# Kernel optimization log

Measured on AMD Instinct MI355X. Metric: run time of the kernel, lower is better.

Reference implementation:

```python
import jax, jax.numpy as jnp
import numpy as np

SPECIES = (0, 1)
CUTOFF = 6.0
N_ATOMS, N_EDGES, N_TRIPLETS = 20000, 500000, 2000000

G2_ETAS = np.array([0.003214, 0.035711, 0.071421, 0.124987, 0.214264, 0.357106, 0.714213, 1.428426], dtype=np.float32)
G4_ETAS = np.array([0.000357, 0.028569, 0.089277], dtype=np.float32)
G4_ZETAS = np.array([1.0, 2.0, 4.0], dtype=np.float32)
G4_LMDAS = np.array([-1.0, 1.0], dtype=np.float32)


def setup_inputs() -> dict:
    key = jax.random.key(0)
    ks = jax.random.split(key, 6)
    atomic_numbers = jax.random.randint(ks[0], (N_ATOMS,), 0, 2, dtype=jnp.int32)
    edge_index = jax.random.randint(ks[1], (2, N_EDGES), 0, N_ATOMS, dtype=jnp.int32)
    D_st = jax.random.uniform(ks[2], (N_EDGES,), minval=0.5, maxval=6.5, dtype=jnp.float32)
    id3_ba = jax.random.randint(ks[3], (N_TRIPLETS,), 0, N_EDGES, dtype=jnp.int32)
    id3_ca = jax.random.randint(ks[4], (N_TRIPLETS,), 0, N_EDGES, dtype=jnp.int32)
    cosphi = jax.random.uniform(ks[5], (N_TRIPLETS,), minval=-1.0, maxval=1.0, dtype=jnp.float32)
    # per-key parameters: 4 ordered species pairs for G2, 6 species triples for G4
    g2_etas = jnp.tile(jnp.asarray(G2_ETAS), (4, 1))
    g4_etas = jnp.tile(jnp.asarray(G4_ETAS), (6, 1))
    g4_zetas = jnp.tile(jnp.asarray(G4_ZETAS), (6, 1))
    g4_lmdas = jnp.tile(jnp.asarray(G4_LMDAS), (6, 1))
    return {"atomic_numbers": atomic_numbers, "edge_index": edge_index, "D_st": D_st,
            "id3_ba": id3_ba, "id3_ca": id3_ca, "cosphi": cosphi,
            "g2_etas": g2_etas, "g4_etas": g4_etas, "g4_zetas": g4_zetas, "g4_lmdas": g4_lmdas}


def _fc(R):
    # cosine cutoff (no in-range bool here; G4 applies its own range masks)
    return 0.5 * jnp.cos(jnp.pi * R / CUTOFF) + 0.5


def _acsf(atomic_numbers, edge_index, D_st, id3_ba, id3_ca, cosphi,
          g2_etas, g4_etas, g4_zetas, g4_lmdas):
    N = atomic_numbers.shape[0]
    dt = D_st.dtype
    src, tgt = edge_index[0], edge_index[1]
    an_src, an_tgt = atomic_numbers[src], atomic_numbers[tgt]

    # ---- triplet geometry (masking replaces boolean gather; scatter-add is equivalent) ----
    m3 = id3_ba > id3_ca                       # [T] triplet dedup mask
    R_ba = D_st[id3_ba]                        # [T]
    R_ca = D_st[id3_ca]
    sb = atomic_numbers[src[id3_ba]]           # species of edge-ba source
    tb = atomic_numbers[tgt[id3_ba]]           # species of central atom a
    sc = atomic_numbers[src[id3_ca]]
    seg3 = tgt[id3_ba]                         # scatter target: central atom index
    Rbc2 = R_ba * R_ba + R_ca * R_ca - 2.0 * R_ba * R_ca * cosphi
    R_bc = jnp.sqrt(jnp.maximum(Rbc2, 1e-12))
    in_range = ((R_bc < CUTOFF) & (R_ba < CUTOFF) & (R_ca < CUTOFF)).astype(dt)
    cut3 = _fc(R_ca) * _fc(R_bc) * _fc(R_ba) * in_range   # [T]
    r2sum = R_bc * R_bc + R_ba * R_ba + R_ca * R_ca       # [T]

    # ---- G2: per (source, target) species pair ----
    cut2 = _fc(D_st)                           # [E]
    d2 = D_st * D_st
    g2_per = {}
    k = 0
    for a1 in SPECIES:
        for a2 in SPECIES:
            w = ((an_tgt == a2) & (an_src == a1)).astype(dt)       # [E]
            res = (cut2 * w)[:, None] * jnp.exp(-g2_etas[k][None, :] * d2[:, None])  # [E,8]
            g2_per[(a1, a2)] = jax.ops.segment_sum(res, tgt, num_segments=N)        # [N,8]
            k += 1

    # ---- G4: per (a, b, c) species triple (b<=c) ----
    ns = len(SPECIES)
    g4_per = {}
    k = 0
    for a in SPECIES:
        for i in range(ns):
            b = SPECIES[i]
            for j in range(i, ns):
                c = SPECIES[j]
                idx = (((sb == b) & (tb == a) & (sc == c)) |
                       ((sb == c) & (tb == a) & (sc == b)))
                w = (m3 & idx).astype(dt)                                  # [T]
                eta, zta, lmda = g4_etas[k], g4_zetas[k], g4_lmdas[k]
                rad = jnp.exp(-eta[None, :] * r2sum[:, None])              # [T,3]
                cl = jnp.abs(1.0 + lmda[None, :, None] * cosphi[:, None, None]) ** zta[None, None, :]  # [T,2,3]
                res = cl[:, None, :, :] * rad[:, :, None, None] * (cut3 * w)[:, None, None, None]      # [T,3,2,3]
                g4 = jax.ops.segment_sum(res, seg3, num_segments=N)        # [N,3,2,3]
                g4_per[(a, b, c)] = (2.0 ** (1.0 - zta))[None, None, None, :] * g4
                k += 1

    # ---- assemble per-atom descriptor [N, 70]; rows carry their species' descriptor ----
    outs = []
    for a in SPECIES:
        mask = (atomic_numbers == a).astype(dt)[:, None]
        g2s = jnp.stack([g2_per[(s, a)] for s in SPECIES], axis=-1).reshape(N, -1)   # [N,16]
        trips = [(b, c) for i, b in enumerate(SPECIES) for c in SPECIES[i:]]
        g4s = jnp.stack([g4_per[(a, b, c)] for (b, c) in trips], axis=-1).reshape(N, -1)  # [N,54]
        outs.append(mask * jnp.concatenate([g2s, g4s], axis=-1))
    return outs[0] + outs[1]


def reference(atomic_numbers, edge_index, D_st, id3_ba, id3_ca, cosphi,
              g2_etas, g4_etas, g4_zetas, g4_lmdas):
    return _acsf(atomic_numbers, edge_index, D_st, id3_ba, id3_ca, cosphi,
                 g2_etas, g4_etas, g4_zetas, g4_lmdas)
```

## Files before the change

kernel.cpp:

```cpp
#include <hip/hip_runtime.h>


#define CAP_T 96
#define CAP_E 64

typedef int    vi2 __attribute__((ext_vector_type(2)));
typedef int    vi4 __attribute__((ext_vector_type(4)));
typedef float  vf2 __attribute__((ext_vector_type(2)));
typedef float  vf4 __attribute__((ext_vector_type(4)));

static __device__ __forceinline__ float fc_dev(float R) {
    const float PI_OVER_CUT = 0.52359877559829887308f;
    return fmaf(0.5f, __cosf(PI_OVER_CUT * R), 0.5f);
}

static __device__ __forceinline__ unsigned enc_R(float d) {
    float u = rintf(d * (65535.0f / 8.0f));
    u = fminf(fmaxf(u, 0.0f), 65535.0f);
    return (unsigned)u;
}
static __device__ __forceinline__ float dec_R(unsigned pk) {
    return (float)(pk >> 16) * (8.0f / 65535.0f);
}


static __device__ __forceinline__ void process_edge(
        int e, float d, int src, int tgt,
        const int* __restrict__ an, const float* __restrict__ g2_etas,
        unsigned* __restrict__ epack, int* __restrict__ ecount,
        unsigned* __restrict__ erec, float* __restrict__ out) {
    int as = an[src];
    unsigned dq = enc_R(d);
    epack[e] = (dq << 16) | ((unsigned)tgt << 1) | (unsigned)as;
    float fcv = fc_dev(d);
    int slot = atomicAdd(&ecount[tgt], 1);
    if (slot < CAP_E) {
        unsigned fq = (unsigned)rintf(fminf(fmaxf(fcv, 0.0f), 1.0f) * 32767.0f);
        erec[(size_t)tgt * CAP_E + slot] = (dq << 16) | (fq << 1) | (unsigned)as;
    } else {
        float d2 = d * d;
        int at = an[tgt];
        const float* eta = g2_etas + (as * 2 + at) * 8;
        float* row = out + (size_t)tgt * 70 + as;
#pragma unroll
        for (int i = 0; i < 8; ++i)
            atomicAdd(row + 2 * i, fcv * __expf(-eta[i] * d2));
    }
}

__global__ void edges_bin_kernel(const int* __restrict__ an,
                                 const int* __restrict__ ei,
                                 const float* __restrict__ D,
                                 const float* __restrict__ g2_etas,
                                 unsigned* __restrict__ epack,
                                 int* __restrict__ ecount,
                                 unsigned* __restrict__ erec,
                                 float* __restrict__ out, int E) {
    int i = blockIdx.x * blockDim.x + threadIdx.x;
    int e0 = i * 2;
    if (e0 >= E) return;
    if (e0 + 1 < E) {
        vi2 sp = __builtin_nontemporal_load((const vi2*)ei + i);
        vi2 tp = __builtin_nontemporal_load((const vi2*)(ei + E) + i);
        vf2 dp = __builtin_nontemporal_load((const vf2*)D + i);
        process_edge(e0,     dp.x, sp.x, tp.x, an, g2_etas, epack, ecount, erec, out);
        process_edge(e0 + 1, dp.y, sp.y, tp.y, an, g2_etas, epack, ecount, erec, out);
    } else {
        process_edge(e0, D[e0], ei[e0], ei[E + e0], an, g2_etas, epack, ecount,
                     erec, out);
    }
}

static __device__ __forceinline__ void process_triplet(
        unsigned pb, unsigned pc, float cph,
        const int* __restrict__ an,
        const float* __restrict__ g4_etas,
        const float* __restrict__ g4_zetas,
        const float* __restrict__ g4_lmdas,
        int* __restrict__ tcount, vf2* __restrict__ trec,
        float* __restrict__ out) {
    float R_ba = dec_R(pb);
    float R_ca = dec_R(pc);
    if (R_ba >= 6.0f || R_ca >= 6.0f) return;
    float Rbc2 = R_ba * R_ba + R_ca * R_ca - 2.0f * R_ba * R_ca * cph;
    float Rm2 = fmaxf(Rbc2, 1e-12f);
    float R_bc = sqrtf(Rm2);
    if (R_bc >= 6.0f) return;
    int seg = (int)((pb >> 1) & 0x7FFFu);
    int trip = (int)(pb & 1u) + (int)(pc & 1u);
    float cut3 = fc_dev(R_ba) * fc_dev(R_ca) * fc_dev(R_bc);
    float r2sum = Rm2 + R_ba * R_ba + R_ca * R_ca;
    int slot = atomicAdd(&tcount[seg], 1);
    if (slot < CAP_T) {
        float cqf = fminf(fmaxf(fmaf(cph, 32767.5f, 32767.5f), 0.0f), 65535.0f);
        unsigned cq = (unsigned)rintf(cqf);
        unsigned c3q = (unsigned)rintf(cut3 * 16383.0f);
        unsigned w0 = (cq << 16) | (c3q << 2) | (unsigned)trip;
        vf2 r; r.x = __uint_as_float(w0); r.y = r2sum;
        trec[(size_t)seg * CAP_T + slot] = r;
    } else {
        int A = an[seg];
        int k4 = A * 3 + trip;
        const float* eta = g4_etas + k4 * 3;
        const float* zet = g4_zetas + k4 * 3;
        const float* lmd = g4_lmdas + k4 * 2;
        float rad[3];
#pragma unroll
        for (int e2 = 0; e2 < 3; ++e2)
            rad[e2] = __expf(-eta[e2] * r2sum) * cut3;
        float lg0 = __log2f(fabsf(fmaf(lmd[0], cph, 1.0f)));
        float lg1 = __log2f(fabsf(fmaf(lmd[1], cph, 1.0f)));
        float* row = out + (size_t)seg * 70 + 16 + trip;
#pragma unroll
        for (int z = 0; z < 3; ++z) {
            float zv = zet[z], base = 1.0f - zv;
            float c0 = exp2f(fmaf(zv, lg0, base));
            float c1 = exp2f(fmaf(zv, lg1, base));
#pragma unroll
            for (int e2 = 0; e2 < 3; ++e2) {
                atomicAdd(row + ((e2 * 2 + 0) * 3 + z) * 3, c0 * rad[e2]);
                atomicAdd(row + ((e2 * 2 + 1) * 3 + z) * 3, c1 * rad[e2]);
            }
        }
    }
}

__global__ void trip_bin_kernel(const unsigned* __restrict__ epack,
                                const int* __restrict__ id3_ba,
                                const int* __restrict__ id3_ca,
                                const float* __restrict__ cosphi,
                                const int* __restrict__ an,
                                const float* __restrict__ g4_etas,
                                const float* __restrict__ g4_zetas,
                                const float* __restrict__ g4_lmdas,
                                int* __restrict__ tcount,
                                vf2* __restrict__ trec,
                                float* __restrict__ out, int T) {
    int i = blockIdx.x * blockDim.x + threadIdx.x;
    int t0 = i * 4;
    if (t0 >= T) return;
    int ba[4], ca[4];
    float cp[4];
    if (t0 + 3 < T) {
        vi4 b4 = __builtin_nontemporal_load((const vi4*)id3_ba + i);
        vi4 c4 = __builtin_nontemporal_load((const vi4*)id3_ca + i);
        vf4 p4 = __builtin_nontemporal_load((const vf4*)cosphi + i);
        ba[0] = b4.x; ba[1] = b4.y; ba[2] = b4.z; ba[3] = b4.w;
        ca[0] = c4.x; ca[1] = c4.y; ca[2] = c4.z; ca[3] = c4.w;
        cp[0] = p4.x; cp[1] = p4.y; cp[2] = p4.z; cp[3] = p4.w;
    } else {
#pragma unroll
        for (int k = 0; k < 4; ++k) {
            int t = t0 + k;
            ba[k] = (t < T) ? id3_ba[t] : 0;
            ca[k] = (t < T) ? id3_ca[t] : 0;
            cp[k] = (t < T) ? cosphi[t] : 0.0f;
        }
    }
    unsigned pb[4], pc[4];
    bool m[4];
#pragma unroll
    for (int k = 0; k < 4; ++k) {
        m[k] = ba[k] > ca[k];
        pb[k] = 0u; pc[k] = 0u;
        if (m[k]) {
            pb[k] = epack[ba[k]];
            pc[k] = epack[ca[k]];
        }
    }
#pragma unroll
    for (int k = 0; k < 4; ++k) {
        if (m[k])
            process_triplet(pb[k], pc[k], cp[k], an, g4_etas, g4_zetas,
                            g4_lmdas, tcount, trec, out);
    }
}

__global__ __launch_bounds__(256) void gather_kernel(
        const int* __restrict__ an,
        const float* __restrict__ g2_etas,
        const float* __restrict__ g4_etas,
        const float* __restrict__ g4_zetas,
        const float* __restrict__ g4_lmdas,
        const int* __restrict__ tcount, const vf2* __restrict__ trec,
        const int* __restrict__ ecount, const unsigned* __restrict__ erec,
        float* __restrict__ out, int N) {
    __shared__ vf2      sg4[4][66];
    __shared__ unsigned sg2[4][64];
    int w = threadIdx.x >> 6;
    int lane = threadIdx.x & 63;
    int a = blockIdx.x * 4 + w;
    if (a >= N) return;
    int A = an[a];

    int c18 = lane % 18;
    int g3  = lane / 18;
    int g3r = (g3 > 2) ? 0 : g3;
    int z_c = c18 % 3;
    int l_c = (c18 / 3) % 2;
    int e_c = c18 / 6;
    float eta0, eta1, eta2w, zv0, zv1, zv2, lm0, lm1, lm2;
    {
        int k0 = A * 3 + 0, k1 = A * 3 + 1, k2 = A * 3 + 2;
        eta0 = g4_etas[k0 * 3 + e_c]; eta1 = g4_etas[k1 * 3 + e_c]; eta2w = g4_etas[k2 * 3 + e_c];
        zv0  = g4_zetas[k0 * 3 + z_c]; zv1 = g4_zetas[k1 * 3 + z_c]; zv2 = g4_zetas[k2 * 3 + z_c];
        lm0  = g4_lmdas[k0 * 2 + l_c]; lm1 = g4_lmdas[k1 * 2 + l_c]; lm2 = g4_lmdas[k2 * 2 + l_c];
    }
    auto zsel = [](float z) -> int {
        return (z == 1.0f) ? 0 : (z == 2.0f) ? 1 : (z == 4.0f) ? 2 : 3;
    };
    int zs0 = zsel(zv0), zs1 = zsel(zv1), zs2 = zsel(zv2);
    bool fastz = __all(zs0 < 3 && zs1 < 3 && zs2 < 3);

    int n_t = min(tcount[a], CAP_T);
    const vf2* rec = trec + (size_t)a * CAP_T;
    float acc0 = 0.0f, acc1 = 0.0f, acc2 = 0.0f;
    vf2 zr; zr.x = 0.0f; zr.y = 0.0f;
    for (int b0 = 0; b0 < n_t; b0 += 64) {
        int nch = min(64, n_t - b0);
        vf2 rv = zr;
        if (lane < nch) rv = __builtin_nontemporal_load(rec + b0 + lane);
        sg4[w][lane] = rv;
        if (lane < 2) sg4[w][64 + lane] = zr;
        asm volatile("s_waitcnt lgkmcnt(0)" ::: "memory");
        int niter = (nch + 2) / 3;
        if (fastz) {
            for (int i = 0; i < niter; ++i) {
                vf2 b = sg4[w][i * 3 + g3r];
                unsigned w0 = __float_as_uint(b.x);
                int btr = (int)(w0 & 3u);
                float cut3 = (float)((w0 >> 2) & 0x3FFFu) * (1.0f / 16383.0f);
                float c = fmaf((float)(w0 >> 16), 2.0f / 65535.0f, -1.0f);
                float eta_r = (btr == 0) ? eta0 : (btr == 1) ? eta1 : eta2w;
                float lm_r  = (btr == 0) ? lm0  : (btr == 1) ? lm1  : lm2;
                int   zs_r  = (btr == 0) ? zs0  : (btr == 1) ? zs1  : zs2;
                float p1 = fabsf(fmaf(lm_r, c, 1.0f));
                float p2 = p1 * p1;
                float p4 = p2 * p2;
                float cl = (zs_r == 0) ? p1 : (zs_r == 1) ? p2 * 0.5f : p4 * 0.125f;
                float v = cl * __expf(-eta_r * b.y) * cut3;
                acc0 += (btr == 0) ? v : 0.0f;
                acc1 += (btr == 1) ? v : 0.0f;
                acc2 += (btr == 2) ? v : 0.0f;
            }
        } else {
            for (int i = 0; i < niter; ++i) {
                vf2 b = sg4[w][i * 3 + g3r];
                unsigned w0 = __float_as_uint(b.x);
                int btr = (int)(w0 & 3u);
                float cut3 = (float)((w0 >> 2) & 0x3FFFu) * (1.0f / 16383.0f);
                float c = fmaf((float)(w0 >> 16), 2.0f / 65535.0f, -1.0f);
                float eta_r = (btr == 0) ? eta0 : (btr == 1) ? eta1 : eta2w;
                float lm_r  = (btr == 0) ? lm0  : (btr == 1) ? lm1  : lm2;
                float zv_r  = (btr == 0) ? zv0  : (btr == 1) ? zv1  : zv2;
                float p1 = fabsf(fmaf(lm_r, c, 1.0f));
                float cl = exp2f(fmaf(zv_r, __log2f(p1), 1.0f - zv_r));
                float v = cl * __expf(-eta_r * b.y) * cut3;
                acc0 += (btr == 0) ? v : 0.0f;
                acc1 += (btr == 1) ? v : 0.0f;
                acc2 += (btr == 2) ? v : 0.0f;
            }
        }
    }
    {
        int cc = lane / 3;
        int tt = lane - cc * 3;
        float s0a = __shfl(acc0, cc),      s1a = __shfl(acc1, cc),      s2a = __shfl(acc2, cc);
        float s0b = __shfl(acc0, cc + 18), s1b = __shfl(acc1, cc + 18), s2b = __shfl(acc2, cc + 18);
        float s0c = __shfl(acc0, cc + 36), s1c = __shfl(acc1, cc + 36), s2c = __shfl(acc2, cc + 36);
        float va = (tt == 0) ? s0a : (tt == 1) ? s1a : s2a;
        float vb = (tt == 0) ? s0b : (tt == 1) ? s1b : s2b;
        float vc = (tt == 0) ? s0c : (tt == 1) ? s1c : s2c;
        if (lane < 54) out[(size_t)a * 70 + 16 + lane] += va + vb + vc;
    }

    int c16 = lane & 15;
    int g4g = lane >> 4;
    int s_c = c16 & 1;
    int i_c = c16 >> 1;
    float eta2 = g2_etas[(s_c * 2 + A) * 8 + i_c];
    int n_e = min(ecount[a], CAP_E);
    const unsigned* erc = erec + (size_t)a * CAP_E;
    float accg = 0.0f;
    for (int b0 = 0; b0 < n_e; b0 += 64) {
        int nch = min(64, n_e - b0);
        unsigned rv = 0u;
        if (lane < nch) rv = __builtin_nontemporal_load(erc + b0 + lane);
        sg2[w][lane] = rv;
        asm volatile("s_waitcnt lgkmcnt(0)" ::: "memory");
        int niter = (nch + 3) / 4;
        for (int i = 0; i < niter; ++i) {
            unsigned pk = sg2[w][i * 4 + g4g];
            int sp = (int)(pk & 1u);
            float d = dec_R(pk);
            float fcv = (float)((pk >> 1) & 0x7FFFu) * (1.0f / 32767.0f);
            float v = fcv * __expf(-eta2 * d * d);
            accg += (sp == s_c) ? v : 0.0f;
        }
    }
    {
        float r0 = __shfl(accg, lane);
        float r1 = __shfl(accg, lane + 16);
        float r2 = __shfl(accg, lane + 32);
        float r3 = __shfl(accg, lane + 48);
        if (lane < 16) out[(size_t)a * 70 + lane] += r0 + r1 + r2 + r3;
    }
}


__global__ void acsf_edges_kernel(const int* __restrict__ an,
                                  const int* __restrict__ ei,
                                  const float* __restrict__ D,
                                  const float* __restrict__ g2_etas,
                                  float2* __restrict__ edata,
                                  float* __restrict__ out,
                                  int E, int use_ws) {
    int e = blockIdx.x * blockDim.x + threadIdx.x;
    if (e >= E) return;
    float d = D[e];
    float cut2 = fc_dev(d);
    if (use_ws) edata[e] = make_float2(d, cut2);
    int src = ei[e];
    int tgt = ei[E + e];
    int as = an[src];
    int at = an[tgt];
    float d2 = d * d;
    const float* eta = g2_etas + (as * 2 + at) * 8;
    float* row = out + (size_t)tgt * 70 + as;
#pragma unroll
    for (int i = 0; i < 8; ++i)
        atomicAdd(row + 2 * i, cut2 * __expf(-eta[i] * d2));
}

__global__ void acsf_triplets_kernel(const int* __restrict__ an,
                                     const int* __restrict__ ei,
                                     const float* __restrict__ D,
                                     const float2* __restrict__ edata,
                                     const int* __restrict__ id3_ba,
                                     const int* __restrict__ id3_ca,
                                     const float* __restrict__ cosphi,
                                     const float* __restrict__ g4_etas,
                                     const float* __restrict__ g4_zetas,
                                     const float* __restrict__ g4_lmdas,
                                     float* __restrict__ out,
                                     int T, int E, int use_ws) {
    int t = blockIdx.x * blockDim.x + threadIdx.x;
    if (t >= T) return;
    int eba = id3_ba[t];
    int eca = id3_ca[t];
    if (eba <= eca) return;
    float R_ba, R_ca, fba, fca;
    if (use_ws) {
        float2 va = edata[eba];
        float2 vb = edata[eca];
        R_ba = va.x; fba = va.y;
        R_ca = vb.x; fca = vb.y;
    } else {
        R_ba = D[eba]; R_ca = D[eca];
        fba = fc_dev(R_ba); fca = fc_dev(R_ca);
    }
    if (R_ba >= 6.0f || R_ca >= 6.0f) return;
    float cph = cosphi[t];
    float Rbc2 = R_ba * R_ba + R_ca * R_ca - 2.0f * R_ba * R_ca * cph;
    float Rm2 = fmaxf(Rbc2, 1e-12f);
    float R_bc = sqrtf(Rm2);
    if (R_bc >= 6.0f) return;
    int seg = ei[E + eba];
    int A = an[seg];
    int sb = an[ei[eba]];
    int sc = an[ei[eca]];
    int trip = sb + sc;
    int k4 = A * 3 + trip;
    float cut3 = fba * fca * fc_dev(R_bc);
    float r2sum = Rm2 + R_ba * R_ba + R_ca * R_ca;
    const float* eta = g4_etas + k4 * 3;
    const float* zet = g4_zetas + k4 * 3;
    const float* lmd = g4_lmdas + k4 * 2;
    float rad[3];
#pragma unroll
    for (int e2 = 0; e2 < 3; ++e2)
        rad[e2] = __expf(-eta[e2] * r2sum) * cut3;
    float lg0 = __log2f(fabsf(fmaf(lmd[0], cph, 1.0f)));
    float lg1 = __log2f(fabsf(fmaf(lmd[1], cph, 1.0f)));
    float* row = out + (size_t)seg * 70 + 16 + trip;
#pragma unroll
    for (int z = 0; z < 3; ++z) {
        float zv = zet[z], bse = 1.0f - zv;
        float c0 = exp2f(fmaf(zv, lg0, bse));
        float c1 = exp2f(fmaf(zv, lg1, bse));
#pragma unroll
        for (int e2 = 0; e2 < 3; ++e2) {
            atomicAdd(row + ((e2 * 2 + 0) * 3 + z) * 3, c0 * rad[e2]);
            atomicAdd(row + ((e2 * 2 + 1) * 3 + z) * 3, c1 * rad[e2]);
        }
    }
}


extern "C" void kernel_launch(void* const* d_in, const int* in_sizes, int n_in,
                              void* d_out, int out_size, void* d_ws, size_t ws_size,
                              hipStream_t stream) {
    const int*   an       = (const int*)d_in[0];
    const int*   ei       = (const int*)d_in[1];
    const float* D        = (const float*)d_in[2];
    const int*   id3_ba   = (const int*)d_in[3];
    const int*   id3_ca   = (const int*)d_in[4];
    const float* cosphi   = (const float*)d_in[5];
    const float* g2_etas  = (const float*)d_in[6];
    const float* g4_etas  = (const float*)d_in[7];
    const float* g4_zetas = (const float*)d_in[8];
    const float* g4_lmdas = (const float*)d_in[9];
    (void)n_in;

    int N = in_sizes[0];
    int E = in_sizes[2];
    int T = in_sizes[3];
    float* out = (float*)d_out;

    size_t trec_b  = (size_t)N * CAP_T * sizeof(vf2);
    size_t epack_b = (size_t)((E + 1) & ~1) * sizeof(unsigned);
    size_t erec_b  = (size_t)N * CAP_E * sizeof(unsigned);
    size_t cnt_b   = (size_t)N * sizeof(int) * 2;
    size_t need = trec_b + epack_b + erec_b + cnt_b;

    const int blk = 256;
    (void)hipMemsetAsync(d_out, 0, (size_t)out_size * sizeof(float), stream);

    if (ws_size >= need && N <= 32767) {
        char* p = (char*)d_ws;
        vf2*      trec  = (vf2*)p;             p += trec_b;
        unsigned* epack = (unsigned*)p;        p += epack_b;
        unsigned* erec  = (unsigned*)p;        p += erec_b;
        int*      tcount = (int*)p;
        int*      ecount = tcount + N;
        (void)hipMemsetAsync(tcount, 0, cnt_b, stream);

        int ethreads = (E + 1) / 2;
        edges_bin_kernel<<<(ethreads + blk - 1) / blk, blk, 0, stream>>>(
            an, ei, D, g2_etas, epack, ecount, erec, out, E);
        int tthreads = (T + 3) / 4;
        trip_bin_kernel<<<(tthreads + blk - 1) / blk, blk, 0, stream>>>(
            epack, id3_ba, id3_ca, cosphi, an,
            g4_etas, g4_zetas, g4_lmdas, tcount, trec, out, T);
        gather_kernel<<<(N + 3) / 4, blk, 0, stream>>>(
            an, g2_etas, g4_etas, g4_zetas, g4_lmdas,
            tcount, trec, ecount, erec, out, N);
    } else {
        int use_ws = (ws_size >= (size_t)E * sizeof(float2)) ? 1 : 0;
        float2* edata = (float2*)d_ws;
        acsf_edges_kernel<<<(E + blk - 1) / blk, blk, 0, stream>>>(
            an, ei, D, g2_etas, edata, out, E, use_ws);
        acsf_triplets_kernel<<<(T + blk - 1) / blk, blk, 0, stream>>>(
            an, ei, D, edata, id3_ba, id3_ca, cosphi,
            g4_etas, g4_zetas, g4_lmdas, out, T, E, use_ws);
    }
}
```

Baseline: 186.6 us.

## Shard per-atom triplet and edge bins across eight block-indexed shards

Splits the per-atom bin counters and record arrays into eight shards chosen by block index, so atomics on the same atom's counter contend less and records spread over more memory. The gather kernel sums the per-shard counts and maps each lane's record index to a shard and local slot before loading. The binning kernels now compute geometry for all four triplets and issue their atomics together to expose more memory-level parallelism. Per-shard capacity is small (16), so more records may spill to the slow direct-atomic path on busy shards. Gather also does eight counter loads and extra index arithmetic per atom.

New measurement: 188.5 us. No clear change (+1.0%).

```diff
diff --git a/kernel.cpp b/kernel.cpp
--- a/kernel.cpp
+++ b/kernel.cpp
@@ -1,13 +1,15 @@
 #include <hip/hip_runtime.h>
 
 
-#define CAP_T 96
-#define CAP_E 64
-
-typedef int    vi2 __attribute__((ext_vector_type(2)));
-typedef int    vi4 __attribute__((ext_vector_type(4)));
-typedef float  vf2 __attribute__((ext_vector_type(2)));
-typedef float  vf4 __attribute__((ext_vector_type(4)));
+#define NSH    8
+#define CAP_TS 16
+#define CAP_ES 16
+
+typedef int      vi2 __attribute__((ext_vector_type(2)));
+typedef int      vi4 __attribute__((ext_vector_type(4)));
+typedef float    vf2 __attribute__((ext_vector_type(2)));
+typedef float    vf4 __attribute__((ext_vector_type(4)));
+typedef unsigned vu2 __attribute__((ext_vector_type(2)));
 
 static __device__ __forceinline__ float fc_dev(float R) {
     const float PI_OVER_CUT = 0.52359877559829887308f;
@@ -23,30 +25,6 @@
     return (float)(pk >> 16) * (8.0f / 65535.0f);
 }
 
-
-static __device__ __forceinline__ void process_edge(
-        int e, float d, int src, int tgt,
-        const int* __restrict__ an, const float* __restrict__ g2_etas,
-        unsigned* __restrict__ epack, int* __restrict__ ecount,
-        unsigned* __restrict__ erec, float* __restrict__ out) {
-    int as = an[src];
-    unsigned dq = enc_R(d);
-    epack[e] = (dq << 16) | ((unsigned)tgt << 1) | (unsigned)as;
-    float fcv = fc_dev(d);
-    int slot = atomicAdd(&ecount[tgt], 1);
-    if (slot < CAP_E) {
-        unsigned fq = (unsigned)rintf(fminf(fmaxf(fcv, 0.0f), 1.0f) * 32767.0f);
-        erec[(size_t)tgt * CAP_E + slot] = (dq << 16) | (fq << 1) | (unsigned)as;
-    } else {
-        float d2 = d * d;
-        int at = an[tgt];
-        const float* eta = g2_etas + (as * 2 + at) * 8;
-        float* row = out + (size_t)tgt * 70 + as;
-#pragma unroll
-        for (int i = 0; i < 8; ++i)
-            atomicAdd(row + 2 * i, fcv * __expf(-eta[i] * d2));
-    }
-}
 
 __global__ void edges_bin_kernel(const int* __restrict__ an,
                                  const int* __restrict__ ei,
@@ -55,72 +33,64 @@
                                  unsigned* __restrict__ epack,
                                  int* __restrict__ ecount,
                                  unsigned* __restrict__ erec,
-                                 float* __restrict__ out, int E) {
+                                 float* __restrict__ out, int E, int N) {
+    int shard = blockIdx.x & (NSH - 1);
+    int* __restrict__ ecnt = ecount + (size_t)shard * N;
     int i = blockIdx.x * blockDim.x + threadIdx.x;
     int e0 = i * 2;
     if (e0 >= E) return;
+
+    int   srcs[2], tgts[2];
+    float ds[2];
+    int   nk;
     if (e0 + 1 < E) {
         vi2 sp = __builtin_nontemporal_load((const vi2*)ei + i);
         vi2 tp = __builtin_nontemporal_load((const vi2*)(ei + E) + i);
         vf2 dp = __builtin_nontemporal_load((const vf2*)D + i);
-        process_edge(e0,     dp.x, sp.x, tp.x, an, g2_etas, epack, ecount, erec, out);
-        process_edge(e0 + 1, dp.y, sp.y, tp.y, an, g2_etas, epack, ecount, erec, out);
+        srcs[0] = sp.x; srcs[1] = sp.y;
+        tgts[0] = tp.x; tgts[1] = tp.y;
+        ds[0] = dp.x;   ds[1] = dp.y;
+        nk = 2;
     } else {
-        process_edge(e0, D[e0], ei[e0], ei[E + e0], an, g2_etas, epack, ecount,
-                     erec, out);
-    }
-}
-
-static __device__ __forceinline__ void process_triplet(
-        unsigned pb, unsigned pc, float cph,
-        const int* __restrict__ an,
-        const float* __restrict__ g4_etas,
-        const float* __restrict__ g4_zetas,
-        const float* __restrict__ g4_lmdas,
-        int* __restrict__ tcount, vf2* __restrict__ trec,
-        float* __restrict__ out) {
-    float R_ba = dec_R(pb);
-    float R_ca = dec_R(pc);
-    if (R_ba >= 6.0f || R_ca >= 6.0f) return;
-    float Rbc2 = R_ba * R_ba + R_ca * R_ca - 2.0f * R_ba * R_ca * cph;
-    float Rm2 = fmaxf(Rbc2, 1e-12f);
-    float R_bc = sqrtf(Rm2);
-    if (R_bc >= 6.0f) return;
-    int seg = (int)((pb >> 1) & 0x7FFFu);
-    int trip = (int)(pb & 1u) + (int)(pc & 1u);
-    float cut3 = fc_dev(R_ba) * fc_dev(R_ca) * fc_dev(R_bc);
-    float r2sum = Rm2 + R_ba * R_ba + R_ca * R_ca;
-    int slot = atomicAdd(&tcount[seg], 1);
-    if (slot < CAP_T) {
-        float cqf = fminf(fmaxf(fmaf(cph, 32767.5f, 32767.5f), 0.0f), 65535.0f);
-        unsigned cq = (unsigned)rintf(cqf);
-        unsigned c3q = (unsigned)rintf(cut3 * 16383.0f);
-        unsigned w0 = (cq << 16) | (c3q << 2) | (unsigned)trip;
-        vf2 r; r.x = __uint_as_float(w0); r.y = r2sum;
-        trec[(size_t)seg * CAP_T + slot] = r;
+        srcs[0] = ei[e0]; tgts[0] = ei[E + e0]; ds[0] = D[e0];
+        srcs[1] = 0;      tgts[1] = 0;          ds[1] = 0.0f;
+        nk = 1;
+    }
+    int as[2];
+#pragma unroll
+    for (int k = 0; k < 2; ++k) as[k] = (k < nk) ? an[srcs[k]] : 0;
+    unsigned pk[2];
+#pragma unroll
+    for (int k = 0; k < 2; ++k)
+        pk[k] = (enc_R(ds[k]) << 16) | ((unsigned)tgts[k] << 1) | (unsigned)as[k];
+    if (nk == 2) {
+        vu2 pv; pv.x = pk[0]; pv.y = pk[1];
+        *((vu2*)epack + i) = pv;
     } else {
-        int A = an[seg];
-        int k4 = A * 3 + trip;
-        const float* eta = g4_etas + k4 * 3;
-        const float* zet = g4_zetas + k4 * 3;
-        const float* lmd = g4_lmdas + k4 * 2;
-        float rad[3];
-#pragma unroll
-        for (int e2 = 0; e2 < 3; ++e2)
-            rad[e2] = __expf(-eta[e2] * r2sum) * cut3;
-        float lg0 = __log2f(fabsf(fmaf(lmd[0], cph, 1.0f)));
-        float lg1 = __log2f(fabsf(fmaf(lmd[1], cph, 1.0f)));
-        float* row = out + (size_t)seg * 70 + 16 + trip;
-#pragma unroll
-        for (int z = 0; z < 3; ++z) {
-            float zv = zet[z], base = 1.0f - zv;
-            float c0 = exp2f(fmaf(zv, lg0, base));
-            float c1 = exp2f(fmaf(zv, lg1, base));
-#pragma unroll
-            for (int e2 = 0; e2 < 3; ++e2) {
-                atomicAdd(row + ((e2 * 2 + 0) * 3 + z) * 3, c0 * rad[e2]);
-                atomicAdd(row + ((e2 * 2 + 1) * 3 + z) * 3, c1 * rad[e2]);
-            }
+        epack[e0] = pk[0];
+    }
+    float fcv[2];
+#pragma unroll
+    for (int k = 0; k < 2; ++k) fcv[k] = fc_dev(ds[k]);
+    int slot[2];
+#pragma unroll
+    for (int k = 0; k < 2; ++k)
+        slot[k] = (k < nk) ? atomicAdd(&ecnt[tgts[k]], 1) : CAP_ES;
+#pragma unroll
+    for (int k = 0; k < 2; ++k) {
+        if (k >= nk) continue;
+        if (slot[k] < CAP_ES) {
+            unsigned fq = (unsigned)rintf(fminf(fmaxf(fcv[k], 0.0f), 1.0f) * 32767.0f);
+            erec[((size_t)shard * N + tgts[k]) * CAP_ES + slot[k]] =
+                (pk[k] & 0xFFFF0000u) | (fq << 1) | (pk[k] & 1u);
+        } else {
+            float d2 = ds[k] * ds[k];
+            int at = an[tgts[k]];
+            const float* eta = g2_etas + (as[k] * 2 + at) * 8;
+            float* row = out + (size_t)tgts[k] * 70 + as[k];
+#pragma unroll
+            for (int q = 0; q < 8; ++q)
+                atomicAdd(row + 2 * q, fcv[k] * __expf(-eta[q] * d2));
         }
     }
 }
@@ -135,10 +105,13 @@
                                 const float* __restrict__ g4_lmdas,
                                 int* __restrict__ tcount,
                                 vf2* __restrict__ trec,
-                                float* __restrict__ out, int T) {
+                                float* __restrict__ out, int T, int N) {
+    int shard = blockIdx.x & (NSH - 1);
+    int* __restrict__ tcnt = tcount + (size_t)shard * N;
     int i = blockIdx.x * blockDim.x + threadIdx.x;
     int t0 = i * 4;
     if (t0 >= T) return;
+
     int ba[4], ca[4];
     float cp[4];
     if (t0 + 3 < T) {
@@ -153,7 +126,7 @@
         for (int k = 0; k < 4; ++k) {
             int t = t0 + k;
             ba[k] = (t < T) ? id3_ba[t] : 0;
-            ca[k] = (t < T) ? id3_ca[t] : 0;
+            ca[k] = (t < T) ? id3_ca[t] : 1;
             cp[k] = (t < T) ? cosphi[t] : 0.0f;
         }
     }
@@ -168,11 +141,62 @@
             pc[k] = epack[ca[k]];
         }
     }
+    float Rba[4], Rca[4], Rm2[4];
+    int seg[4];
+    bool valid[4];
 #pragma unroll
     for (int k = 0; k < 4; ++k) {
-        if (m[k])
-            process_triplet(pb[k], pc[k], cp[k], an, g4_etas, g4_zetas,
-                            g4_lmdas, tcount, trec, out);
+        Rba[k] = dec_R(pb[k]);
+        Rca[k] = dec_R(pc[k]);
+        float Rbc2 = Rba[k] * Rba[k] + Rca[k] * Rca[k]
+                     - 2.0f * Rba[k] * Rca[k] * cp[k];
+        Rm2[k] = fmaxf(Rbc2, 1e-12f);
+        float Rbc = sqrtf(Rm2[k]);
+        valid[k] = m[k] && (Rba[k] < 6.0f) && (Rca[k] < 6.0f) && (Rbc < 6.0f);
+        seg[k] = (int)((pb[k] >> 1) & 0x7FFFu);
+    }
+    int slot[4];
+#pragma unroll
+    for (int k = 0; k < 4; ++k)
+        slot[k] = valid[k] ? atomicAdd(&tcnt[seg[k]], 1) : CAP_TS;
+#pragma unroll
+    for (int k = 0; k < 4; ++k) {
+        if (!valid[k]) continue;
+        float r2sum = Rm2[k] + Rba[k] * Rba[k] + Rca[k] * Rca[k];
+        float cut3 = fc_dev(Rba[k]) * fc_dev(Rca[k]) * fc_dev(sqrtf(Rm2[k]));
+        int trip = (int)(pb[k] & 1u) + (int)(pc[k] & 1u);
+        if (slot[k] < CAP_TS) {
+            float cqf = fminf(fmaxf(fmaf(cp[k], 32767.5f, 32767.5f), 0.0f), 65535.0f);
+            unsigned cq = (unsigned)rintf(cqf);
+            unsigned c3q = (unsigned)rintf(cut3 * 16383.0f);
+            unsigned w0 = (cq << 16) | (c3q << 2) | (unsigned)trip;
+            vf2 r; r.x = __uint_as_float(w0); r.y = r2sum;
+            trec[((size_t)shard * N + seg[k]) * CAP_TS + slot[k]] = r;
+        } else {
+            int A = an[seg[k]];
+            int k4 = A * 3 + trip;
+            const float* eta = g4_etas + k4 * 3;
+            const float* zet = g4_zetas + k4 * 3;
+            const float* lmd = g4_lmdas + k4 * 2;
+            float rad[3];
+#pragma unroll
+            for (int e2 = 0; e2 < 3; ++e2)
+                rad[e2] = __expf(-eta[e2] * r2sum) * cut3;
+            float lg0 = __log2f(fabsf(fmaf(lmd[0], cp[k], 1.0f)));
+            float lg1 = __log2f(fabsf(fmaf(lmd[1], cp[k], 1.0f)));
+            float* row = out + (size_t)seg[k] * 70 + 16 + trip;
+#pragma unroll
+            for (int z = 0; z < 3; ++z) {
+                float zv = zet[z], base = 1.0f - zv;
+                float c0 = exp2f(fmaf(zv, lg0, base));
+                float c1 = exp2f(fmaf(zv, lg1, base));
+#pragma unroll
+                for (int e2 = 0; e2 < 3; ++e2) {
+                    atomicAdd(row + ((e2 * 2 + 0) * 3 + z) * 3, c0 * rad[e2]);
+                    atomicAdd(row + ((e2 * 2 + 1) * 3 + z) * 3, c1 * rad[e2]);
+                }
+            }
+        }
     }
 }
 
@@ -212,14 +236,31 @@
     int zs0 = zsel(zv0), zs1 = zsel(zv1), zs2 = zsel(zv2);
     bool fastz = __all(zs0 < 3 && zs1 < 3 && zs2 < 3);
 
-    int n_t = min(tcount[a], CAP_T);
-    const vf2* rec = trec + (size_t)a * CAP_T;
+    int tcnt_[NSH];
+#pragma unroll
+    for (int q = 0; q < NSH; ++q)
+        tcnt_[q] = min(tcount[(size_t)q * N + a], CAP_TS);
+    int n_t = 0;
+#pragma unroll
+    for (int q = 0; q < NSH; ++q) n_t += tcnt_[q];
+
     float acc0 = 0.0f, acc1 = 0.0f, acc2 = 0.0f;
     vf2 zr; zr.x = 0.0f; zr.y = 0.0f;
     for (int b0 = 0; b0 < n_t; b0 += 64) {
         int nch = min(64, n_t - b0);
         vf2 rv = zr;
-        if (lane < nch) rv = __builtin_nontemporal_load(rec + b0 + lane);
+        if (lane < nch) {
+            int loc = b0 + lane, s = 0;
+            bool done = false;
+#pragma unroll
+            for (int q = 0; q < NSH - 1; ++q) {
+                bool go = !done && (loc >= tcnt_[q]);
+                loc  = go ? loc - tcnt_[q] : loc;
+                s   += go ? 1 : 0;
+                done = !go;
+            }
+            rv = trec[((size_t)s * N + a) * CAP_TS + loc];
+        }
         sg4[w][lane] = rv;
         if (lane < 2) sg4[w][64 + lane] = zr;
         asm volatile("s_waitcnt lgkmcnt(0)" ::: "memory");
@@ -279,13 +320,30 @@
     int s_c = c16 & 1;
     int i_c = c16 >> 1;
     float eta2 = g2_etas[(s_c * 2 + A) * 8 + i_c];
-    int n_e = min(ecount[a], CAP_E);
-    const unsigned* erc = erec + (size_t)a * CAP_E;
+    int ecnt_[NSH];
+#pragma unroll
+    for (int q = 0; q < NSH; ++q)
+        ecnt_[q] = min(ecount[(size_t)q * N + a], CAP_ES);
+    int n_e = 0;
+#pragma unroll
+    for (int q = 0; q < NSH; ++q) n_e += ecnt_[q];
+
     float accg = 0.0f;
     for (int b0 = 0; b0 < n_e; b0 += 64) {
         int nch = min(64, n_e - b0);
         unsigned rv = 0u;
-        if (lane < nch) rv = __builtin_nontemporal_load(erc + b0 + lane);
+        if (lane < nch) {
+            int loc = b0 + lane, s = 0;
+            bool done = false;
+#pragma unroll
+            for (int q = 0; q < NSH - 1; ++q) {
+                bool go = !done && (loc >= ecnt_[q]);
+                loc  = go ? loc - ecnt_[q] : loc;
+                s   += go ? 1 : 0;
+                done = !go;
+            }
+            rv = erec[((size_t)s * N + a) * CAP_ES + loc];
+        }
         sg2[w][lane] = rv;
         asm volatile("s_waitcnt lgkmcnt(0)" ::: "memory");
         int niter = (nch + 3) / 4;
@@ -417,11 +475,11 @@
     int T = in_sizes[3];
     float* out = (float*)d_out;
 
-    size_t trec_b  = (size_t)N * CAP_T * sizeof(vf2);
-    size_t epack_b = (size_t)((E + 1) & ~1) * sizeof(unsigned);
-    size_t erec_b  = (size_t)N * CAP_E * sizeof(unsigned);
-    size_t cnt_b   = (size_t)N * sizeof(int) * 2;
-    size_t need = trec_b + epack_b + erec_b + cnt_b;
+    size_t trec_b  = (size_t)NSH * N * CAP_TS * sizeof(vf2);
+    size_t erec_b  = (size_t)NSH * N * CAP_ES * sizeof(unsigned);
+    size_t epack_b = (size_t)((E + 3) & ~3) * sizeof(unsigned);
+    size_t cnt_b   = (size_t)2 * NSH * N * sizeof(int);
+    size_t need = trec_b + erec_b + epack_b + cnt_b;
 
     const int blk = 256;
     (void)hipMemsetAsync(d_out, 0, (size_t)out_size * sizeof(float), stream);
@@ -429,19 +487,19 @@
     if (ws_size >= need && N <= 32767) {
         char* p = (char*)d_ws;
         vf2*      trec  = (vf2*)p;             p += trec_b;
+        unsigned* erec  = (unsigned*)p;        p += erec_b;
         unsigned* epack = (unsigned*)p;        p += epack_b;
-        unsigned* erec  = (unsigned*)p;        p += erec_b;
         int*      tcount = (int*)p;
-        int*      ecount = tcount + N;
+        int*      ecount = tcount + (size_t)NSH * N;
         (void)hipMemsetAsync(tcount, 0, cnt_b, stream);
 
         int ethreads = (E + 1) / 2;
         edges_bin_kernel<<<(ethreads + blk - 1) / blk, blk, 0, stream>>>(
-            an, ei, D, g2_etas, epack, ecount, erec, out, E);
+            an, ei, D, g2_etas, epack, ecount, erec, out, E, N);
         int tthreads = (T + 3) / 4;
         trip_bin_kernel<<<(tthreads + blk - 1) / blk, blk, 0, stream>>>(
             epack, id3_ba, id3_ca, cosphi, an,
-            g4_etas, g4_zetas, g4_lmdas, tcount, trec, out, T);
+            g4_etas, g4_zetas, g4_lmdas, tcount, trec, out, T, N);
         gather_kernel<<<(N + 3) / 4, blk, 0, stream>>>(
             an, g2_etas, g4_etas, g4_zetas, g4_lmdas,
             tcount, trec, ecount, erec, out, N);
```
